# Kernel optimization log

Hardware: AMD Instinct MI355X
Metric: run time of the kernel (lower is better)

Reference implementation:

```python
import jax, jax.numpy as jnp
import numpy as np

D_MODEL = 256
NUM_HEAD = 4
D_HEAD = D_MODEL // NUM_HEAD
B, N, M = 1, 512, 512


def setup_inputs() -> dict:
    key = jax.random.key(0)
    ks = jax.random.split(key, 13)
    s = 1.0 / np.sqrt(D_MODEL)
    inp = {
        'input_q': jax.random.normal(ks[0], (B, N, D_MODEL), jnp.float32),
        'input_k': jax.random.normal(ks[1], (B, M, D_MODEL), jnp.float32),
        'input_v': jax.random.normal(ks[2], (B, M, D_MODEL), jnp.float32),
        'input_p': jax.random.normal(ks[3], (B, N, M, D_MODEL), jnp.float32),
        'key_masks': jnp.zeros((B, M), dtype=bool),
        'Wq': jax.random.normal(ks[4], (D_MODEL, D_MODEL), jnp.float32) * s,
        'bq': jnp.zeros((D_MODEL,), jnp.float32),
        'Wk': jax.random.normal(ks[5], (D_MODEL, D_MODEL), jnp.float32) * s,
        'bk': jnp.zeros((D_MODEL,), jnp.float32),
        'Wv': jax.random.normal(ks[6], (D_MODEL, D_MODEL), jnp.float32) * s,
        'bv': jnp.zeros((D_MODEL,), jnp.float32),
        'Wp': jax.random.normal(ks[7], (D_MODEL, D_MODEL), jnp.float32) * s,
        'bp': jnp.zeros((D_MODEL,), jnp.float32),
    }
    return inp


def reference(input_q, input_k, input_v, input_p, key_masks,
              Wq, bq, Wk, bk, Wv, bv, Wp, bp):
    H, Dh = NUM_HEAD, D_HEAD
    b, n, _ = input_q.shape
    m = input_k.shape[1]
    # linear projections (PyTorch Linear: x @ W.T + b)
    q = (input_q @ Wq.T + bq).reshape(b, n, H, Dh).transpose(0, 2, 1, 3)   # (B,H,N,Dh)
    k = (input_k @ Wk.T + bk).reshape(b, m, H, Dh).transpose(0, 2, 1, 3)   # (B,H,M,Dh)
    v = (input_v @ Wv.T + bv).reshape(b, m, H, Dh).transpose(0, 2, 1, 3)   # (B,H,M,Dh)
    p = (input_p @ Wp.T + bp).reshape(b, n, m, H, Dh)                      # (B,N,M,H,Dh)
    # content scores + per-pair RPE scores (q dot p)
    scores = (jnp.einsum('bhnd,bhmd->bhnm', q, k)
              + jnp.einsum('bhnd,bnmhd->bhnm', q, p)) / np.sqrt(Dh)
    scores = jnp.where(key_masks[:, None, None, :], -jnp.inf, scores)
    attn = jax.nn.softmax(scores, axis=-1)                                 # (B,H,N,M)
    hidden = jnp.einsum('bhnm,bhmd->bhnd', attn, v)
    hidden = hidden.transpose(0, 2, 1, 3).reshape(b, n, H * Dh)            # (B,N,C)
    return hidden
```

## Files before the change

### kernel.cpp

```cpp
#include <hip/hip_runtime.h>
#include <math.h>

#define DMODEL 256
#define NSEQ   512
#define MSEQ   512

#define WS_Q      0
#define WS_K      131072
#define WS_V      262144
#define WS_WPE    393216
#define WS_SQK    917504

typedef float v4f __attribute__((ext_vector_type(4)));

__global__ __launch_bounds__(256) void proj_qkv(
    const float* __restrict__ xq, const float* __restrict__ xk,
    const float* __restrict__ xv,
    const float* __restrict__ Wq, const float* __restrict__ bq,
    const float* __restrict__ Wk, const float* __restrict__ bk,
    const float* __restrict__ Wv, const float* __restrict__ bv,
    float* __restrict__ ws)
{
    int bid = blockIdx.x;
    int mat = bid >> 6;
    int rb  = bid & 63;
    const float* X; const float* W; const float* b; float* Y;
    if (mat == 0)      { X = xq; W = Wq; b = bq; Y = ws + WS_Q; }
    else if (mat == 1) { X = xk; W = Wk; b = bk; Y = ws + WS_K; }
    else               { X = xv; W = Wv; b = bv; Y = ws + WS_V; }

    int c  = threadIdx.x;
    int r0 = rb * 8;
    float acc[8];
    float bias = b[c];
#pragma unroll
    for (int r = 0; r < 8; ++r) acc[r] = bias;

    const float4* Wrow = (const float4*)(W + (size_t)c * DMODEL);
    for (int d4 = 0; d4 < 64; ++d4) {
        float4 w = Wrow[d4];
#pragma unroll
        for (int r = 0; r < 8; ++r) {
            float4 x = ((const float4*)(X + (size_t)(r0 + r) * DMODEL))[d4];
            acc[r] += w.x * x.x + w.y * x.y + w.z * x.z + w.w * x.w;
        }
    }
#pragma unroll
    for (int r = 0; r < 8; ++r)
        Y[(size_t)(r0 + r) * DMODEL + c] = acc[r];
}

__global__ __launch_bounds__(256) void make_wpeff(
    const float* __restrict__ Wp, float* __restrict__ ws)
{
    const float* q   = ws + WS_Q;
    float*       wpe = ws + WS_WPE;
    int n = blockIdx.x;
    int d = threadIdx.x;

    __shared__ float ql[256];
    ql[d] = q[(size_t)n * DMODEL + d];
    __syncthreads();

    float acc[4];
#pragma unroll
    for (int h = 0; h < 4; ++h) {
        float a = 0.f;
#pragma unroll 8
        for (int dh = 0; dh < 64; ++dh) {
            int c = h * 64 + dh;
            a += ql[c] * Wp[(size_t)c * DMODEL + d];
        }
        acc[h] = a;
    }
    *(float4*)&wpe[(size_t)n * 1024 + d * 4] =
        make_float4(acc[0], acc[1], acc[2], acc[3]);
}

__global__ __launch_bounds__(256) void qk_scores(
    const float* __restrict__ bp, float* __restrict__ ws)
{
    const float* q   = ws + WS_Q;
    const float* k   = ws + WS_K;
    float*       sqk = ws + WS_SQK;

    int bid = blockIdx.x;
    int h   = bid >> 6;
    int g   = bid & 63;
    int n0  = g * 8;
    int tid = threadIdx.x;

    __shared__ float qls[8][64];
    __shared__ float qb[8];

    if (tid < 128) {
        int row = tid >> 4, col = (tid & 15) * 4;
        *(float4*)&qls[row][col] =
            *(const float4*)&q[(size_t)(n0 + row) * DMODEL + h * 64 + col];
    }
    __syncthreads();
    if (tid < 8) {
        float s = 0.f;
        for (int dh = 0; dh < 64; ++dh) s += qls[tid][dh] * bp[h * 64 + dh];
        qb[tid] = s;
    }
    __syncthreads();

    const float* ka = k + (size_t)tid * DMODEL + h * 64;
    const float* kb = ka + (size_t)256 * DMODEL;
    float acca[8] = {};
    float accb[8] = {};
#pragma unroll 4
    for (int d4 = 0; d4 < 16; ++d4) {
        float4 xa = *(const float4*)(ka + d4 * 4);
        float4 xb = *(const float4*)(kb + d4 * 4);
#pragma unroll
        for (int j = 0; j < 8; ++j) {
            float4 qq = *(const float4*)&qls[j][d4 * 4];
            acca[j] += xa.x * qq.x + xa.y * qq.y + xa.z * qq.z + xa.w * qq.w;
            accb[j] += xb.x * qq.x + xb.y * qq.y + xb.z * qq.z + xb.w * qq.w;
        }
    }
#pragma unroll
    for (int j = 0; j < 8; ++j) {
        size_t base = (size_t)h * 262144 + (size_t)(n0 + j) * MSEQ;
        sqk[base + tid]       = 0.125f * (acca[j] + qb[j]);
        sqk[base + tid + 256] = 0.125f * (accb[j] + qb[j]);
    }
}

__global__ __launch_bounds__(256) void p_scores(
    const float* __restrict__ Xp, float* __restrict__ ws)
{
    const float* wpe = ws + WS_WPE;
    float*       sqk = ws + WS_SQK;

    int bid  = blockIdx.x;
    int n    = bid >> 1;
    int m0   = (bid & 1) * 256;
    int tid  = threadIdx.x;
    int wv   = tid >> 6;
    int lane = tid & 63;
    int p    = lane & 15;
    int r3   = lane >> 4;

    const float4* wp4 = (const float4*)(wpe + (size_t)n * 1024);
    float4 w[4][4];
#pragma unroll
    for (int j = 0; j < 4; ++j)
#pragma unroll
        for (int c = 0; c < 4; ++c)
            w[j][c] = wp4[4 * p + 64 * j + c];

    __shared__ float sm[4][256];

    const v4f* base4 =
        (const v4f*)Xp + ((size_t)n * MSEQ + m0 + wv * 64) * 64;

#pragma unroll 2
    for (int g = 0; g < 16; ++g) {
        int rbase = (g * 4 + r3) * 64 + p;
        v4f xv0 = __builtin_nontemporal_load(&base4[rbase + 0]);
        v4f xv1 = __builtin_nontemporal_load(&base4[rbase + 16]);
        v4f xv2 = __builtin_nontemporal_load(&base4[rbase + 32]);
        v4f xv3 = __builtin_nontemporal_load(&base4[rbase + 48]);

        float sh[4] = {0.f, 0.f, 0.f, 0.f};
        {
            const v4f xs[4] = {xv0, xv1, xv2, xv3};
#pragma unroll
            for (int j = 0; j < 4; ++j) {
#pragma unroll
                for (int c = 0; c < 4; ++c) {
                    const float xc = xs[j][c];
                    const float* wf = &w[j][c].x;
#pragma unroll
                    for (int h = 0; h < 4; ++h)
                        sh[h] += xc * wf[h];
                }
            }
        }
#pragma unroll
        for (int off = 1; off < 16; off <<= 1) {
#pragma unroll
            for (int h = 0; h < 4; ++h)
                sh[h] += __shfl_xor(sh[h], off);
        }
        if (p == 0) {
            int ml = wv * 64 + g * 4 + r3;
            sm[0][ml] = sh[0];
            sm[1][ml] = sh[1];
            sm[2][ml] = sh[2];
            sm[3][ml] = sh[3];
        }
    }
    __syncthreads();

    size_t ob = (size_t)n * MSEQ + m0 + tid;
#pragma unroll
    for (int h = 0; h < 4; ++h)
        sqk[h * 262144 + ob] += 0.125f * sm[h][tid];
}

__global__ __launch_bounds__(256) void softmax_av(
    const unsigned char* __restrict__ mask,
    float* __restrict__ out, float* __restrict__ ws)
{
    const float* v      = ws + WS_V;
    const float* scores = ws + WS_SQK;

    int bid = blockIdx.x;
    int h   = bid >> 6;
    int g   = bid & 63;
    int n0  = g * 8;

    __shared__ float  pl[MSEQ * 8];
    __shared__ float4 red4[256];
    __shared__ float  wred[4];

    int tid  = threadIdx.x;
    int lane = tid & 63, wv = tid >> 6;

    for (int j = 0; j < 8; ++j) {
        int n = n0 + j;
        const float* srow = scores + (size_t)h * 262144 + (size_t)n * MSEQ;
        float s0 = srow[tid];
        float s1 = srow[tid + 256];
        if (mask[tid])       s0 = -INFINITY;
        if (mask[tid + 256]) s1 = -INFINITY;

        float mx = fmaxf(s0, s1);
#pragma unroll
        for (int off = 32; off; off >>= 1) mx = fmaxf(mx, __shfl_xor(mx, off));
        if (lane == 0) wred[wv] = mx;
        __syncthreads();
        mx = fmaxf(fmaxf(wred[0], wred[1]), fmaxf(wred[2], wred[3]));

        float e0 = __expf(s0 - mx);
        float e1 = __expf(s1 - mx);
        float sm = e0 + e1;
#pragma unroll
        for (int off = 32; off; off >>= 1) sm += __shfl_xor(sm, off);
        __syncthreads();
        if (lane == 0) wred[wv] = sm;
        __syncthreads();
        sm = wred[0] + wred[1] + wred[2] + wred[3];
        float rinv = 1.0f / sm;

        pl[(size_t)tid * 8 + j]         = e0 * rinv;
        pl[(size_t)(tid + 256) * 8 + j] = e1 * rinv;
        __syncthreads();
    }

    int dhq = tid & 15, mq = tid >> 4;
    float acc[8][4] = {};
    for (int i = 0; i < 32; ++i) {
        int m = mq * 32 + i;
        float4 vv = *(const float4*)&v[(size_t)m * DMODEL + h * 64 + dhq * 4];
        float4 pa = *(const float4*)&pl[m * 8];
        float4 pb = *(const float4*)&pl[m * 8 + 4];
#pragma unroll
        for (int j = 0; j < 4; ++j) {
            float pv = (&pa.x)[j];
            acc[j][0] += pv * vv.x; acc[j][1] += pv * vv.y;
            acc[j][2] += pv * vv.z; acc[j][3] += pv * vv.w;
        }
#pragma unroll
        for (int j = 0; j < 4; ++j) {
            float pv = (&pb.x)[j];
            acc[4 + j][0] += pv * vv.x; acc[4 + j][1] += pv * vv.y;
            acc[4 + j][2] += pv * vv.z; acc[4 + j][3] += pv * vv.w;
        }
    }

    for (int j = 0; j < 8; ++j) {
        red4[mq * 16 + dhq] =
            make_float4(acc[j][0], acc[j][1], acc[j][2], acc[j][3]);
        __syncthreads();
        if (tid < 64) {
            int dq = tid >> 2, x = tid & 3;
            float s = 0.f;
#pragma unroll
            for (int qq = 0; qq < 16; ++qq)
                s += ((const float*)&red4[qq * 16 + dq])[x];
            out[(size_t)(n0 + j) * DMODEL + h * 64 + tid] = s;
        }
        __syncthreads();
    }
}

extern "C" void kernel_launch(void* const* d_in, const int* in_sizes, int n_in,
                              void* d_out, int out_size, void* d_ws,
                              size_t ws_size, hipStream_t stream)
{
    const float* xq = (const float*)d_in[0];
    const float* xk = (const float*)d_in[1];
    const float* xv = (const float*)d_in[2];
    const float* xp = (const float*)d_in[3];
    const unsigned char* mask = (const unsigned char*)d_in[4];
    const float* Wq = (const float*)d_in[5];
    const float* bq = (const float*)d_in[6];
    const float* Wk = (const float*)d_in[7];
    const float* bk = (const float*)d_in[8];
    const float* Wv = (const float*)d_in[9];
    const float* bv = (const float*)d_in[10];
    const float* Wp = (const float*)d_in[11];
    const float* bp = (const float*)d_in[12];
    float* out = (float*)d_out;
    float* ws  = (float*)d_ws;

    proj_qkv  <<<192,  256, 0, stream>>>(xq, xk, xv, Wq, bq, Wk, bk, Wv, bv, ws);
    make_wpeff<<<512,  256, 0, stream>>>(Wp, ws);
    qk_scores <<<256,  256, 0, stream>>>(bp, ws);
    p_scores  <<<1024, 256, 0, stream>>>(xp, ws);
    softmax_av<<<256,  256, 0, stream>>>(mask, out, ws);
}
```

Baseline: 107.9 us.

## Assign one full P row per thread with LDS-broadcast weights in p_scores

Restructures the RPE score kernel so each thread reads an entire 256-float row of input_p and computes all four head scores itself. The folded weights go into shared memory and are broadcast, which removes the cross-lane shuffle reductions and the shared-memory staging of partial sums. The row is loaded in double-buffered register chunks. In exchange, a wavefront's loads become strided by a full row per lane instead of contiguous, nontemporal hints are dropped, and register pressure rises.

```diff
diff --git a/kernel.cpp b/kernel.cpp
--- a/kernel.cpp
+++ b/kernel.cpp
@@ -135,71 +135,54 @@
     const float* wpe = ws + WS_WPE;
     float*       sqk = ws + WS_SQK;
 
-    int bid  = blockIdx.x;
-    int n    = bid >> 1;
-    int m0   = (bid & 1) * 256;
-    int tid  = threadIdx.x;
-    int wv   = tid >> 6;
-    int lane = tid & 63;
-    int p    = lane & 15;
-    int r3   = lane >> 4;
-
-    const float4* wp4 = (const float4*)(wpe + (size_t)n * 1024);
-    float4 w[4][4];
-#pragma unroll
-    for (int j = 0; j < 4; ++j)
-#pragma unroll
-        for (int c = 0; c < 4; ++c)
-            w[j][c] = wp4[4 * p + 64 * j + c];
-
-    __shared__ float sm[4][256];
-
-    const v4f* base4 =
-        (const v4f*)Xp + ((size_t)n * MSEQ + m0 + wv * 64) * 64;
-
-#pragma unroll 2
-    for (int g = 0; g < 16; ++g) {
-        int rbase = (g * 4 + r3) * 64 + p;
-        v4f xv0 = __builtin_nontemporal_load(&base4[rbase + 0]);
-        v4f xv1 = __builtin_nontemporal_load(&base4[rbase + 16]);
-        v4f xv2 = __builtin_nontemporal_load(&base4[rbase + 32]);
-        v4f xv3 = __builtin_nontemporal_load(&base4[rbase + 48]);
-
-        float sh[4] = {0.f, 0.f, 0.f, 0.f};
-        {
-            const v4f xs[4] = {xv0, xv1, xv2, xv3};
-#pragma unroll
-            for (int j = 0; j < 4; ++j) {
-#pragma unroll
-                for (int c = 0; c < 4; ++c) {
-                    const float xc = xs[j][c];
-                    const float* wf = &w[j][c].x;
-#pragma unroll
-                    for (int h = 0; h < 4; ++h)
-                        sh[h] += xc * wf[h];
-                }
-            }
-        }
-#pragma unroll
-        for (int off = 1; off < 16; off <<= 1) {
-#pragma unroll
-            for (int h = 0; h < 4; ++h)
-                sh[h] += __shfl_xor(sh[h], off);
-        }
-        if (p == 0) {
-            int ml = wv * 64 + g * 4 + r3;
-            sm[0][ml] = sh[0];
-            sm[1][ml] = sh[1];
-            sm[2][ml] = sh[2];
-            sm[3][ml] = sh[3];
-        }
-    }
+    int n = blockIdx.x >> 1;
+    int m = (blockIdx.x & 1) * 256 + threadIdx.x;
+
+    __shared__ float4 wl[256];
+    wl[threadIdx.x] = ((const float4*)(wpe + (size_t)n * 1024))[threadIdx.x];
     __syncthreads();
 
-    size_t ob = (size_t)n * MSEQ + m0 + tid;
-#pragma unroll
-    for (int h = 0; h < 4; ++h)
-        sqk[h * 262144 + ob] += 0.125f * sm[h][tid];
+    const v4f* __restrict__ xrow =
+        (const v4f*)(Xp + ((size_t)n * MSEQ + m) * DMODEL);
+
+    v4f xa[16], xb[16];
+#pragma unroll
+    for (int i = 0; i < 16; ++i) xa[i] = xrow[i];
+#pragma unroll
+    for (int i = 0; i < 16; ++i) xb[i] = xrow[16 + i];
+
+    float s0 = 0.f, s1 = 0.f, s2 = 0.f, s3 = 0.f;
+
+    auto consume = [&](const v4f* cur, int base) {
+#pragma unroll
+        for (int i = 0; i < 16; ++i) {
+            int d4 = base + i;
+            v4f x = cur[i];
+            float4 w0 = wl[d4 * 4 + 0];
+            float4 w1 = wl[d4 * 4 + 1];
+            float4 w2 = wl[d4 * 4 + 2];
+            float4 w3 = wl[d4 * 4 + 3];
+            s0 += x.x * w0.x + x.y * w1.x + x.z * w2.x + x.w * w3.x;
+            s1 += x.x * w0.y + x.y * w1.y + x.z * w2.y + x.w * w3.y;
+            s2 += x.x * w0.z + x.y * w1.z + x.z * w2.z + x.w * w3.z;
+            s3 += x.x * w0.w + x.y * w1.w + x.z * w2.w + x.w * w3.w;
+        }
+    };
+
+    consume(xa, 0);
+#pragma unroll
+    for (int i = 0; i < 16; ++i) xa[i] = xrow[32 + i];
+    consume(xb, 16);
+#pragma unroll
+    for (int i = 0; i < 16; ++i) xb[i] = xrow[48 + i];
+    consume(xa, 32);
+    consume(xb, 48);
+
+    size_t ob = (size_t)n * MSEQ + m;
+    sqk[0 * 262144 + ob] += 0.125f * s0;
+    sqk[1 * 262144 + ob] += 0.125f * s1;
+    sqk[2 * 262144 + ob] += 0.125f * s2;
+    sqk[3 * 262144 + ob] += 0.125f * s3;
 }
 
 __global__ __launch_bounds__(256) void softmax_av(
```

Measured after the change: 119.6 us. 1.11x slower.
